# Optimization experiments

Hardware: AMD Instinct MI355X
Metric: run time of the kernel (lower is better)

## Reference

```python
import jax, jax.numpy as jnp
import numpy as np

d = 1024
D = 8388608            # number of target params
LL = 1 << int(np.ceil(np.log2(D)))  # = 2**23 = D (power of two)


def fwht(x):
    """Unnormalized Fast Walsh-Hadamard Transform of a length-2^k vector.

    Matches fast_walsh_hadamard_torched(..., normalize=False): butterflies on
    each bit (sum/diff), all bit-stages commute so ordering is irrelevant.
    """
    n = x.shape[0]
    h = 1
    while h < n:
        x = x.reshape(n // (2 * h), 2, h)
        x = jnp.stack([x[:, 0] + x[:, 1], x[:, 0] - x[:, 1]], axis=1)
        h *= 2
    return x.reshape(n)


def setup_inputs() -> dict:
    key = jax.random.key(0)
    k1, k2, k3, k4 = jax.random.split(key, 4)
    x = jax.random.normal(k1, (d,), dtype=jnp.float32)
    # BB: random +/-1 signs (torch.randint(0,2)*2-1)
    BB = (jax.random.randint(k2, (LL,), 0, 2) * 2 - 1).astype(jnp.float32)
    # Pi: random permutation of [0, LL)
    Pi = jax.random.permutation(k3, LL)
    # GG: standard normal gains
    GG = jax.random.normal(k4, (LL,), dtype=jnp.float32)
    return {"x": x, "BB": BB, "GG": GG, "Pi": Pi}


def reference(x, BB, GG, Pi):
    # pad x from d up to LL with zeros
    d_pad = jnp.zeros((LL,), dtype=x.dtype).at[: x.shape[0]].set(x)
    mul_1 = BB * d_pad            # diagonal sign scale
    mul_2 = fwht(mul_1)           # first Hadamard butterfly
    mul_3 = mul_2[Pi]             # permutation gather
    mul_4 = mul_3 * GG            # diagonal Gaussian scale
    return fwht(mul_4)            # second Hadamard butterfly
```

## Files before the change

### kernel.cpp

```cpp
#include <hip/hip_runtime.h>


#define LOWC 16384
#define NC   16384
#define TRPAD 260

__device__ __forceinline__ void fwht64(float* v) {
  #pragma unroll
  for (int s = 0; s < 6; ++s) {
    const int d = 1 << s;
    #pragma unroll
    for (int jj = 0; jj < 64; ++jj) {
      if ((jj & d) == 0) {
        float a = v[jj], b = v[jj + d];
        v[jj]     = a + b;
        v[jj + d] = a - b;
      }
    }
  }
}

__global__ __launch_bounds__(256) void k_low(
    const float* __restrict__ x, const float* __restrict__ BB,
    const int* __restrict__ Pi, const float* __restrict__ GG,
    float* __restrict__ out)
{
  __shared__ float w[1024];
  __shared__ float tr[32 * TRPAD];
  const int t = threadIdx.x;
  const long base = (long)blockIdx.x * LOWC;

  {
    float4 xx = ((const float4*)x)[t];
    float4 bb = ((const float4*)BB)[t];
    float a0 = xx.x * bb.x, a1 = xx.y * bb.y, a2 = xx.z * bb.z, a3 = xx.w * bb.w;
    float b0 = a0 + a1, b1 = a0 - a1, b2 = a2 + a3, b3 = a2 - a3;
    w[4 * t + 0] = b0 + b2; w[4 * t + 1] = b1 + b3;
    w[4 * t + 2] = b0 - b2; w[4 * t + 3] = b1 - b3;
  }
  __syncthreads();
  #pragma unroll
  for (int s = 2; s <= 9; ++s) {
    const int h = 1 << s;
    #pragma unroll
    for (int k2 = 0; k2 < 2; ++k2) {
      int jb = k2 * 256 + t;
      int i0 = ((jb >> s) << (s + 1)) | (jb & (h - 1));
      float aa = w[i0], bv = w[i0 + h];
      w[i0] = aa + bv; w[i0 + h] = aa - bv;
    }
    __syncthreads();
  }

  float v[64];
  {
    const int4*   Pi4 = (const int4*)(Pi + base);
    const float4* GG4 = (const float4*)(GG + base);
    const int vbase = (t >> 2) * 64 + (t & 3);
    #pragma unroll
    for (int q = 0; q < 16; ++q) {
      int4   p = Pi4[vbase + q * 4];
      float4 g = GG4[vbase + q * 4];
      v[4 * q + 0] = w[p.x & 1023] * g.x;
      v[4 * q + 1] = w[p.y & 1023] * g.y;
      v[4 * q + 2] = w[p.z & 1023] * g.z;
      v[4 * q + 3] = w[p.w & 1023] * g.w;
    }
  }

  fwht64(v);

  #pragma unroll
  for (int jj = 0; jj < 64; ++jj) {
    float u = __shfl_xor(v[jj], 1);
    v[jj] = (t & 1) ? (u - v[jj]) : (v[jj] + u);
  }
  #pragma unroll
  for (int jj = 0; jj < 64; ++jj) {
    float u = __shfl_xor(v[jj], 2);
    v[jj] = (t & 2) ? (u - v[jj]) : (v[jj] + u);
  }

  float nv[64];
  #pragma unroll
  for (int r = 0; r < 2; ++r) {
    if (r == 1) __syncthreads();
    #pragma unroll
    for (int jl = 0; jl < 32; ++jl)
      tr[jl * TRPAD + t] = v[r * 32 + jl];
    __syncthreads();
    if ((t >> 7) == r) {
      const int jl = (((t >> 4) << 2) | (t & 3)) & 31;
      const int cc = (t >> 2) & 3;
      #pragma unroll
      for (int j2 = 0; j2 < 64; ++j2)
        nv[j2] = tr[jl * TRPAD + j2 * 4 + cc];
    }
  }

  fwht64(nv);

  #pragma unroll
  for (int j2 = 0; j2 < 64; ++j2)
    out[base + (long)j2 * 256 + t] = nv[j2];
}

__global__ __launch_bounds__(256) void k_high(float* __restrict__ out)
{
  __shared__ float tr[32 * TRPAD];
  const int t = threadIdx.x;
  const long cb = (long)blockIdx.x * 32;
  const int c = t & 31;
  const int g = t >> 5;

  float v[64];
  #pragma unroll
  for (int j = 0; j < 64; ++j)
    v[j] = out[(long)(j * 8 + g) * NC + cb + c];

  fwht64(v);

  float nv[64];
  #pragma unroll
  for (int r = 0; r < 2; ++r) {
    if (r == 1) __syncthreads();
    #pragma unroll
    for (int jl = 0; jl < 32; ++jl)
      tr[jl * TRPAD + t] = v[r * 32 + jl];
    __syncthreads();
    if ((t >> 7) == r) {
      #pragma unroll
      for (int j2 = 0; j2 < 64; ++j2) {
        int jl = ((g & 3) * 8) + (j2 >> 3);
        nv[j2] = tr[jl * TRPAD + ((j2 & 7) << 5) + c];
      }
    }
  }

  #pragma unroll
  for (int s = 0; s < 3; ++s) {
    const int d = 1 << s;
    #pragma unroll
    for (int jj = 0; jj < 64; ++jj) {
      if ((jj & d) == 0) {
        float a = nv[jj], b = nv[jj + d];
        nv[jj]     = a + b;
        nv[jj + d] = a - b;
      }
    }
  }

  #pragma unroll
  for (int j2 = 0; j2 < 64; ++j2)
    out[(long)(g * 64 + j2) * NC + cb + c] = nv[j2];
}

extern "C" void kernel_launch(void* const* d_in, const int* in_sizes, int n_in,
                              void* d_out, int out_size, void* d_ws, size_t ws_size,
                              hipStream_t stream) {
  const float* x  = (const float*)d_in[0];
  const float* BB = (const float*)d_in[1];
  const float* GG = (const float*)d_in[2];
  const int*   Pi = (const int*)  d_in[3];
  float* out = (float*)d_out;

  const int nchunks = (1 << 23) / LOWC;
  k_low<<<nchunks, 256, 0, stream>>>(x, BB, Pi, GG, out);

  const int ntiles = NC / 32;
  k_high<<<ntiles, 256, 0, stream>>>(out);
}
```

Baseline: 139.4 us.

## Store intermediate Hadamard result in bf16 workspace and prefetch Pi early

The intermediate array between the two kernels is now written to a bf16 workspace buffer instead of fp32 in the output, which halves the write and read-back traffic of that large intermediate. Pi indices are also loaded into registers before the shared-memory FWHT, so their global latency overlaps the first transform. The bf16 rounding of the intermediate lowers accuracy and may exceed tolerance. The early Pi prefetch adds 64 live registers per thread, which can reduce occupancy.

```diff
diff --git a/kernel.cpp b/kernel.cpp
--- a/kernel.cpp
+++ b/kernel.cpp
@@ -1,8 +1,8 @@
 #include <hip/hip_runtime.h>
+#include <hip/hip_bf16.h>
 
 
-#define LOWC 16384
-#define NC   16384
+#define NC 16384
 #define TRPAD 260
 
 __device__ __forceinline__ void fwht64(float* v) {
@@ -23,12 +23,20 @@
 __global__ __launch_bounds__(256) void k_low(
     const float* __restrict__ x, const float* __restrict__ BB,
     const int* __restrict__ Pi, const float* __restrict__ GG,
-    float* __restrict__ out)
+    __hip_bfloat16* __restrict__ mid)
 {
   __shared__ float w[1024];
   __shared__ float tr[32 * TRPAD];
   const int t = threadIdx.x;
-  const long base = (long)blockIdx.x * LOWC;
+  const long base = (long)blockIdx.x * NC;
+
+  const int4*   Pi4 = (const int4*)(Pi + base);
+  const float4* GG4 = (const float4*)(GG + base);
+  const int vb = (t >> 2) * 64 + (t & 3);
+
+  int4 p[16];
+  #pragma unroll
+  for (int q = 0; q < 16; ++q) p[q] = Pi4[vb + 4 * q];
 
   {
     float4 xx = ((const float4*)x)[t];
@@ -53,19 +61,13 @@
   }
 
   float v[64];
-  {
-    const int4*   Pi4 = (const int4*)(Pi + base);
-    const float4* GG4 = (const float4*)(GG + base);
-    const int vbase = (t >> 2) * 64 + (t & 3);
-    #pragma unroll
-    for (int q = 0; q < 16; ++q) {
-      int4   p = Pi4[vbase + q * 4];
-      float4 g = GG4[vbase + q * 4];
-      v[4 * q + 0] = w[p.x & 1023] * g.x;
-      v[4 * q + 1] = w[p.y & 1023] * g.y;
-      v[4 * q + 2] = w[p.z & 1023] * g.z;
-      v[4 * q + 3] = w[p.w & 1023] * g.w;
-    }
+  #pragma unroll
+  for (int q = 0; q < 16; ++q) {
+    float4 g = GG4[vb + 4 * q];
+    v[4 * q + 0] = w[p[q].x & 1023] * g.x;
+    v[4 * q + 1] = w[p[q].y & 1023] * g.y;
+    v[4 * q + 2] = w[p[q].z & 1023] * g.z;
+    v[4 * q + 3] = w[p[q].w & 1023] * g.w;
   }
 
   fwht64(v);
@@ -102,21 +104,22 @@
 
   #pragma unroll
   for (int j2 = 0; j2 < 64; ++j2)
-    out[base + (long)j2 * 256 + t] = nv[j2];
+    mid[base + j2 * 256 + t] = __float2bfloat16(nv[j2]);
 }
 
-__global__ __launch_bounds__(256) void k_high(float* __restrict__ out)
+__global__ __launch_bounds__(256) void k_high(
+    const __hip_bfloat16* __restrict__ mid, float* __restrict__ out)
 {
   __shared__ float tr[32 * TRPAD];
   const int t = threadIdx.x;
   const long cb = (long)blockIdx.x * 32;
   const int c = t & 31;
-  const int g = t >> 5;
+  const int g2 = t >> 5;
 
   float v[64];
   #pragma unroll
   for (int j = 0; j < 64; ++j)
-    v[j] = out[(long)(j * 8 + g) * NC + cb + c];
+    v[j] = __bfloat162float(mid[(long)(j * 8 + g2) * NC + cb + c]);
 
   fwht64(v);
 
@@ -131,7 +134,7 @@
     if ((t >> 7) == r) {
       #pragma unroll
       for (int j2 = 0; j2 < 64; ++j2) {
-        int jl = ((g & 3) * 8) + (j2 >> 3);
+        int jl = ((g2 & 3) * 8) + (j2 >> 3);
         nv[j2] = tr[jl * TRPAD + ((j2 & 7) << 5) + c];
       }
     }
@@ -152,7 +155,7 @@
 
   #pragma unroll
   for (int j2 = 0; j2 < 64; ++j2)
-    out[(long)(g * 64 + j2) * NC + cb + c] = nv[j2];
+    out[(long)(g2 * 64 + j2) * NC + cb + c] = nv[j2];
 }
 
 extern "C" void kernel_launch(void* const* d_in, const int* in_sizes, int n_in,
@@ -163,10 +166,8 @@
   const float* GG = (const float*)d_in[2];
   const int*   Pi = (const int*)  d_in[3];
   float* out = (float*)d_out;
+  __hip_bfloat16* mid = (__hip_bfloat16*)d_ws;
 
-  const int nchunks = (1 << 23) / LOWC;
-  k_low<<<nchunks, 256, 0, stream>>>(x, BB, Pi, GG, out);
-
-  const int ntiles = NC / 32;
-  k_high<<<ntiles, 256, 0, stream>>>(out);
+  k_low<<<512, 256, 0, stream>>>(x, BB, Pi, GG, mid);
+  k_high<<<512, 256, 0, stream>>>(mid, out);
 }
```

Result: faster. 136.5 us (-2.1%).
